# Kernel optimization log

Hardware: AMD Instinct MI355X
Metric: run time of the kernel (lower is better)

Reference implementation:

```python
import jax, jax.numpy as jnp
import numpy as np
import math

D_MODEL = 64
N_HEAD = 8
BATCH = 16
NTOK = 511  # pads to 512 in original torch code; padn = 1 > 0


def setup_inputs() -> dict:
    key = jax.random.key(0)
    ks = jax.random.split(key, 4)
    scl = 0.005
    x = jax.random.normal(ks[0], (BATCH, NTOK, D_MODEL), jnp.float32)
    wq_w = scl * jax.random.normal(ks[1], (N_HEAD * D_MODEL, D_MODEL + 1), jnp.float32)
    wq_w = wq_w.at[:, -1].set(0.0)  # bias column zeroed at init
    wv_w = scl * jax.random.normal(ks[2], (N_HEAD * D_MODEL, D_MODEL + 1), jnp.float32)
    wv_w = wv_w.at[:, -1].set(0.0)
    wk = scl * jnp.ones((N_HEAD, D_MODEL), jnp.float32)
    fanout_w = scl * jax.random.normal(ks[3], (D_MODEL, D_MODEL + 1), jnp.float32)
    fanout_w = fanout_w.at[:, -1].set(0.0)
    return {"x": x, "wq_w": wq_w, "wv_w": wv_w, "wk": wk, "fanout_w": fanout_w}


def _linear_m(w, x):
    # LinearM: w[:, :-1] is weight, w[:, -1] is bias
    return jnp.einsum('oi,bti->bto', w[:, :-1], x) + w[:, -1]


def _l1_logits(q, k):
    # q, k: [b, t, h, w]. Returns [b, s(key), d(query), h] =
    #   -(1/sqrt(w)) * sum_w |q[b,d,h,w] - k[b,s,h,w]|
    # Scan over the width axis so we never materialize a [b,t,t,h,w] tensor.
    b, t, h, w = q.shape
    scale = 1.0 / math.sqrt(w)
    qw = jnp.moveaxis(q, -1, 0)  # [w, b, t, h]
    kw = jnp.moveaxis(k, -1, 0)

    def body(acc, qk):
        qi, ki = qk  # each [b, t, h]
        return acc + jnp.abs(qi[:, None, :, :] - ki[:, :, None, :]), None

    acc0 = jnp.zeros((b, t, t, h), q.dtype)
    acc, _ = jax.lax.scan(body, acc0, (qw, kw))
    return -acc * scale


def reference(x, wq_w, wv_w, wk, fanout_w):
    b, t, dm = x.shape
    q = _linear_m(wq_w, x).reshape(b, t, N_HEAD, D_MODEL)
    v = _linear_m(wv_w, x).reshape(b, t, N_HEAD, D_MODEL)
    # k: x broadcast over heads, elementwise-gated by wk
    k = x[:, :, None, :] * wk[None, None, :, :]  # [b, t, h, w]
    logits = _l1_logits(q, k)  # [b, s, d, h]
    # Extra zero-logit 'sink' key row (the original zero-padded row with a[:,t,:,:]=0)
    sink = jnp.zeros((b, 1, t, N_HEAD), logits.dtype)
    logits = jnp.concatenate([logits, sink], axis=1)  # [b, t+1, d, h]
    a = jax.nn.softmax(logits, axis=1)[:, :t]  # softmax over keys+sink, drop sink
    # einsum 'bsdh,bshw->bdhw' then sum over h, fused:
    out = jnp.einsum('bsdh,bshw->bdw', a, v)  # [b, t, d_model]
    y = jax.nn.relu(out)  # module's self.gelu is actually nn.ReLU()
    y = _linear_m(fanout_w, y)
    return x + y
```

## Files before the change

kernel.cpp:

```cpp
#include <hip/hip_runtime.h>
#include <stdint.h>


#define B  16
#define H  8
#define T  511

typedef __fp16 f16x2 __attribute__((ext_vector_type(2)));
typedef __fp16 f16x8 __attribute__((ext_vector_type(8)));
typedef float  f32x4 __attribute__((ext_vector_type(4)));

#if __has_builtin(__builtin_amdgcn_exp2f)
#define EXP2F(x) __builtin_amdgcn_exp2f(x)
#else
#define EXP2F(x) exp2f(x)
#endif

__device__ __forceinline__ uint32_t SAD(uint32_t a, uint32_t b, uint32_t c) {
#if __has_builtin(__builtin_amdgcn_sad_u8)
  return __builtin_amdgcn_sad_u8(a, b, c);
#else
  uint32_t d;
  asm("v_sad_u8 %0, %1, %2, %3" : "=v"(d) : "v"(a), "v"(b), "v"(c));
  return d;
#endif
}

__device__ __forceinline__ uint32_t PKRTZ(float a, float b) {
  f16x2 r = __builtin_amdgcn_cvt_pkrtz(a, b);
  return __builtin_bit_cast(uint32_t, r);
}

__device__ __forceinline__ uint32_t quantu8(float v) {
  float q = __builtin_rintf(__builtin_fmaf(v, 256.f, 128.f));
  q = fminf(fmaxf(q, 0.f), 255.f);
  return (uint32_t)(int)q;
}

__global__ void wtrans_kernel(const float* __restrict__ wq, const float* __restrict__ wv,
                              const float* __restrict__ wf, float* __restrict__ wt,
                              float* __restrict__ bias, float* __restrict__ wft,
                              float* __restrict__ biasf) {
  const int idx = blockIdx.x * 256 + (int)threadIdx.x;
  if (idx < 64 * 1024) {
    const int k = idx >> 10, j = idx & 1023;
    const float* src = (j < 512) ? wq : wv;
    const int oc = j & 511;
    wt[idx] = src[oc * 65 + k];
    if (k == 0) bias[j] = src[oc * 65 + 64];
  } else if (idx < 64 * 1024 + 64 * 64) {
    const int r = idx - 64 * 1024;
    const int k = r >> 6, w = r & 63;
    wft[r] = wf[w * 65 + k];
    if (k == 0) biasf[w] = wf[w * 65 + 64];
  }
}

__global__ void __launch_bounds__(256, 2) proj_kernel(
    const float* __restrict__ x, const float* __restrict__ wt,
    const float* __restrict__ bias, const float* __restrict__ wk,
    uint8_t* __restrict__ qq, _Float16* __restrict__ vt,
    uint8_t* __restrict__ kq) {
  __shared__ float xt[64][16];
  const int b = blockIdx.y, tc = blockIdx.x;
  const int t0 = tc * 16;
  const int tid = threadIdx.x;
  {
    const int tl = tid >> 4, k0 = (tid & 15) * 4;
    const int t = t0 + tl;
    float4 v = {0.f, 0.f, 0.f, 0.f};
    if (t < T) v = *(const float4*)(x + ((size_t)b * T + t) * 64 + k0);
    xt[k0 + 0][tl] = v.x; xt[k0 + 1][tl] = v.y;
    xt[k0 + 2][tl] = v.z; xt[k0 + 3][tl] = v.w;
  }
  __syncthreads();
  const int j0 = tid * 4;
  const float4 bs = *(const float4*)(bias + j0);
  float4 acc[16];
#pragma unroll
  for (int t = 0; t < 16; ++t) acc[t] = bs;
  for (int k = 0; k < 64; ++k) {
    const float4 w4 = *(const float4*)(wt + (size_t)k * 1024 + j0);
    const float4* xr = (const float4*)xt[k];
    const float4 xa = xr[0], xb = xr[1], xc = xr[2], xd = xr[3];
    const float xv[16] = {xa.x, xa.y, xa.z, xa.w, xb.x, xb.y, xb.z, xb.w,
                          xc.x, xc.y, xc.z, xc.w, xd.x, xd.y, xd.z, xd.w};
#pragma unroll
    for (int t = 0; t < 16; ++t) {
      acc[t].x = __builtin_fmaf(w4.x, xv[t], acc[t].x);
      acc[t].y = __builtin_fmaf(w4.y, xv[t], acc[t].y);
      acc[t].z = __builtin_fmaf(w4.z, xv[t], acc[t].z);
      acc[t].w = __builtin_fmaf(w4.w, xv[t], acc[t].w);
    }
  }
  const int oc = j0 & 511;
  const int hh = oc >> 6, w0 = oc & 63;
  const size_t bh = (size_t)b * H + hh;
  if (j0 < 512) {
#pragma unroll
    for (int t = 0; t < 16; ++t) {
      if (t0 + t < T) {
        const uint32_t u = quantu8(acc[t].x) | (quantu8(acc[t].y) << 8) |
                           (quantu8(acc[t].z) << 16) | (quantu8(acc[t].w) << 24);
        *(uint32_t*)(qq + (bh * T + (size_t)(t0 + t)) * 64 + w0) = u;
      }
    }
  } else {
#pragma unroll
    for (int i = 0; i < 4; ++i) {
      uint32_t u[8];
      const float* a = (const float*)acc;
#pragma unroll
      for (int m = 0; m < 8; ++m) u[m] = PKRTZ(a[4 * (2 * m) + i], a[4 * (2 * m + 1) + i]);
      _Float16* p = vt + (bh * 64 + (size_t)(w0 + i)) * 512 + t0;
      *(uint4*)(p)     = make_uint4(u[0], u[1], u[2], u[3]);
      *(uint4*)(p + 8) = make_uint4(u[4], u[5], u[6], u[7]);
    }
  }
  const int tk = tid >> 4, w4 = (tid & 15) * 4;
  if (t0 + tk < T) {
    const float xv0 = xt[w4 + 0][tk], xv1 = xt[w4 + 1][tk];
    const float xv2 = xt[w4 + 2][tk], xv3 = xt[w4 + 3][tk];
#pragma unroll
    for (int hh2 = 0; hh2 < H; ++hh2) {
      const float4 wkv = *(const float4*)(wk + hh2 * 64 + w4);
      const uint32_t u = quantu8(xv0 * wkv.x) | (quantu8(xv1 * wkv.y) << 8) |
                         (quantu8(xv2 * wkv.z) << 16) | (quantu8(xv3 * wkv.w) << 24);
      *(uint32_t*)(kq + (((size_t)b * H + hh2) * T + (size_t)(t0 + tk)) * 64 + w4) = u;
    }
  }
}

__global__ void __launch_bounds__(256, 1) attn_kernel(
    const uint8_t* __restrict__ qq, const uint8_t* __restrict__ kq,
    const _Float16* __restrict__ vt, _Float16* __restrict__ anum) {
  __shared__ uint4 klds[2048];
  const int qt = blockIdx.x, h = blockIdx.y, b = blockIdx.z;
  const int bh = b * H + h;
  const int tid = threadIdx.x;
  {
    const uint4* kg = (const uint4*)(kq + (size_t)bh * T * 64);
    for (int i = tid; i < T * 4; i += 256) {
      const int s = i >> 2, j = i & 3;
      klds[s * 4 + (j ^ ((s >> 3) & 3))] = kg[i];
    }
  }
  const int wave = tid >> 6, lane = tid & 63;
  const int c = lane & 15, g = lane >> 4;
  const int qb = qt * 256 + wave * 64;
  uint4 q[4][4];
#pragma unroll
  for (int m = 0; m < 4; ++m) {
    const int qm = qb + 16 * m + c;
    const int qsafe = qm < T ? qm : T - 1;
    const uint4* qp = (const uint4*)(qq + ((size_t)bh * T + qsafe) * 64);
#pragma unroll
    for (int i = 0; i < 4; ++i) q[m][i] = qp[i];
  }
  const _Float16* vb = vt + (size_t)bh * 64 * 512;
  f32x4 acc[4][4];
#pragma unroll
  for (int m = 0; m < 4; ++m)
#pragma unroll
    for (int nt = 0; nt < 4; ++nt) acc[m][nt] = f32x4{0.f, 0.f, 0.f, 0.f};
  float den[4] = {0.f, 0.f, 0.f, 0.f};
  const float Cl = -0x1.715476p+0f / 2048.0f;
  __syncthreads();

#pragma unroll 1
  for (int kt = 0; kt < 16; ++kt) {
    const int ks = kt * 32;
    const _Float16* vp0 = vb + (size_t)c * 512 + ks + g * 8;
    uint4 bvec[4];
#pragma unroll
    for (int nt = 0; nt < 4; ++nt) bvec[nt] = *(const uint4*)(vp0 + nt * 16 * 512);
    uint32_t pk[4][4];
#pragma unroll
    for (int jj = 0; jj < 4; ++jj) {
      float pp[4][2];
#pragma unroll
      for (int e = 0; e < 2; ++e) {
        const int s = ks + g * 8 + jj * 2 + e;
        const int sr = s < T ? s : T - 1;
        const uint4* kp = klds + sr * 4;
        const int bb = (sr >> 3) & 3;
        const uint4 k0 = kp[bb], k1 = kp[1 ^ bb], k2 = kp[2 ^ bb], k3 = kp[3 ^ bb];
        const bool live = s < T;
#pragma unroll
        for (int m = 0; m < 4; ++m) {
          uint32_t a0 = 0, a1 = 0;
          a0 = SAD(q[m][0].x, k0.x, a0); a0 = SAD(q[m][0].y, k0.y, a0);
          a0 = SAD(q[m][0].z, k0.z, a0); a0 = SAD(q[m][0].w, k0.w, a0);
          a0 = SAD(q[m][1].x, k1.x, a0); a0 = SAD(q[m][1].y, k1.y, a0);
          a0 = SAD(q[m][1].z, k1.z, a0); a0 = SAD(q[m][1].w, k1.w, a0);
          a1 = SAD(q[m][2].x, k2.x, a1); a1 = SAD(q[m][2].y, k2.y, a1);
          a1 = SAD(q[m][2].z, k2.z, a1); a1 = SAD(q[m][2].w, k2.w, a1);
          a1 = SAD(q[m][3].x, k3.x, a1); a1 = SAD(q[m][3].y, k3.y, a1);
          a1 = SAD(q[m][3].z, k3.z, a1); a1 = SAD(q[m][3].w, k3.w, a1);
          const float p = EXP2F((float)(a0 + a1) * Cl);
          pp[m][e] = live ? p : 0.f;
        }
      }
#pragma unroll
      for (int m = 0; m < 4; ++m) {
        den[m] += pp[m][0] + pp[m][1];
        pk[m][jj] = PKRTZ(pp[m][0], pp[m][1]);
      }
    }
#pragma unroll
    for (int m = 0; m < 4; ++m) {
      const f16x8 af = __builtin_bit_cast(f16x8, make_uint4(pk[m][0], pk[m][1], pk[m][2], pk[m][3]));
#pragma unroll
      for (int nt = 0; nt < 4; ++nt) {
        const f16x8 bf = __builtin_bit_cast(f16x8, bvec[nt]);
        acc[m][nt] = __builtin_amdgcn_mfma_f32_16x16x32_f16(af, bf, acc[m][nt], 0, 0, 0);
      }
    }
  }

#pragma unroll
  for (int m = 0; m < 4; ++m) {
    den[m] += __shfl_xor(den[m], 16, 64);
    den[m] += __shfl_xor(den[m], 32, 64);
    den[m] += 1.0f;
  }
#pragma unroll
  for (int m = 0; m < 4; ++m) {
#pragma unroll
    for (int r = 0; r < 4; ++r) {
      const float rd = 1.0f / __shfl(den[m], g * 4 + r, 64);
      const int qr = qb + 16 * m + g * 4 + r;
      if (qr < T) {
        _Float16* ap = anum + (((size_t)b * T + qr) * H + h) * 64 + c;
        ap[0]  = (_Float16)(acc[m][0][r] * rd);
        ap[16] = (_Float16)(acc[m][1][r] * rd);
        ap[32] = (_Float16)(acc[m][2][r] * rd);
        ap[48] = (_Float16)(acc[m][3][r] * rd);
      }
    }
  }
}

__global__ void __launch_bounds__(256) finalize_kernel(
    const float* __restrict__ x, const _Float16* __restrict__ anum,
    const float* __restrict__ wft, const float* __restrict__ biasf,
    float* __restrict__ out) {
  __shared__ float u[4][64];
  const int tid = threadIdx.x;
  const int lt = tid >> 6, w = tid & 63;
  const int gt = blockIdx.x * 4 + lt;
  const _Float16* an = anum + (size_t)gt * H * 64 + w;
  float s = 0.f;
#pragma unroll
  for (int hh = 0; hh < H; ++hh) s += (float)an[hh * 64];
  u[lt][w] = fmaxf(s, 0.f);
  __syncthreads();
  float y = biasf[w];
#pragma unroll 8
  for (int k = 0; k < 64; ++k) y = __builtin_fmaf(wft[k * 64 + w], u[lt][k], y);
  out[(size_t)gt * 64 + w] = x[(size_t)gt * 64 + w] + y;
}

extern "C" void kernel_launch(void* const* d_in, const int* in_sizes, int n_in,
                              void* d_out, int out_size, void* d_ws, size_t ws_size,
                              hipStream_t stream) {
  (void)in_sizes; (void)n_in; (void)out_size; (void)ws_size;
  const float* x  = (const float*)d_in[0];
  const float* wq = (const float*)d_in[1];
  const float* wv = (const float*)d_in[2];
  const float* wk = (const float*)d_in[3];
  const float* wf = (const float*)d_in[4];
  float* out = (float*)d_out;

  uint8_t* ws = (uint8_t*)d_ws;
  const size_t o_qq   = 0;
  const size_t o_kq   = 4186112;
  const size_t o_vt   = 8372224;
  const size_t o_anum = 16760832;
  const size_t o_wt   = 25133056;
  const size_t o_bias = 25395200;
  const size_t o_wft  = 25399296;
  const size_t o_bf   = 25415680;

  uint8_t*  qq    = ws + o_qq;
  uint8_t*  kq    = ws + o_kq;
  _Float16* vt    = (_Float16*)(ws + o_vt);
  _Float16* anum  = (_Float16*)(ws + o_anum);
  float*    wt    = (float*)(ws + o_wt);
  float*    bias  = (float*)(ws + o_bias);
  float*    wft   = (float*)(ws + o_wft);
  float*    biasf = (float*)(ws + o_bf);

  wtrans_kernel<<<dim3((64 * 1024 + 64 * 64 + 255) / 256), 256, 0, stream>>>(
      wq, wv, wf, wt, bias, wft, biasf);
  proj_kernel<<<dim3(32, B), 256, 0, stream>>>(x, wt, bias, wk, qq, vt, kq);
  attn_kernel<<<dim3(2, H, B), 256, 0, stream>>>(qq, kq, vt, anum);
  finalize_kernel<<<dim3(B * T / 4), 256, 0, stream>>>(x, anum, wft, biasf, out);
}
```

Before: 76.52 us.

## Split attention key range across two wave groups with LDS partial-sum reduction

Doubles the attention block to 512 threads. Two wave groups handle the same query rows, each over half of the key range, and their partial numerators and denominators are combined through LDS. The grid is only 256 blocks on a machine with many CUs, so each CU had just 4 waves; this raises the wave count per block so more latency can be hidden. In exchange it adds an LDS reduction, two extra barriers, and fp16 rounding of the partial accumulators.

New measurement: 77.97 us. No clear change (+1.9%).

```diff
diff --git a/kernel.cpp b/kernel.cpp
--- a/kernel.cpp
+++ b/kernel.cpp
@@ -131,23 +131,25 @@
   }
 }
 
-__global__ void __launch_bounds__(256, 1) attn_kernel(
+__global__ void __launch_bounds__(512, 2) attn_kernel(
     const uint8_t* __restrict__ qq, const uint8_t* __restrict__ kq,
     const _Float16* __restrict__ vt, _Float16* __restrict__ anum) {
   __shared__ uint4 klds[2048];
+  __shared__ float dend[4][4][16];
   const int qt = blockIdx.x, h = blockIdx.y, b = blockIdx.z;
   const int bh = b * H + h;
   const int tid = threadIdx.x;
   {
     const uint4* kg = (const uint4*)(kq + (size_t)bh * T * 64);
-    for (int i = tid; i < T * 4; i += 256) {
+    for (int i = tid; i < T * 4; i += 512) {
       const int s = i >> 2, j = i & 3;
       klds[s * 4 + (j ^ ((s >> 3) & 3))] = kg[i];
     }
   }
   const int wave = tid >> 6, lane = tid & 63;
+  const int pair = wave & 3, khalf = wave >> 2;
   const int c = lane & 15, g = lane >> 4;
-  const int qb = qt * 256 + wave * 64;
+  const int qb = qt * 256 + pair * 64;
   uint4 q[4][4];
 #pragma unroll
   for (int m = 0; m < 4; ++m) {
@@ -168,8 +170,8 @@
   __syncthreads();
 
 #pragma unroll 1
-  for (int kt = 0; kt < 16; ++kt) {
-    const int ks = kt * 32;
+  for (int kt = 0; kt < 8; ++kt) {
+    const int ks = khalf * 256 + kt * 32;
     const _Float16* vp0 = vb + (size_t)c * 512 + ks + g * 8;
     uint4 bvec[4];
 #pragma unroll
@@ -222,20 +224,51 @@
   for (int m = 0; m < 4; ++m) {
     den[m] += __shfl_xor(den[m], 16, 64);
     den[m] += __shfl_xor(den[m], 32, 64);
-    den[m] += 1.0f;
-  }
-#pragma unroll
-  for (int m = 0; m < 4; ++m) {
-#pragma unroll
-    for (int r = 0; r < 4; ++r) {
-      const float rd = 1.0f / __shfl(den[m], g * 4 + r, 64);
-      const int qr = qb + 16 * m + g * 4 + r;
-      if (qr < T) {
-        _Float16* ap = anum + (((size_t)b * T + qr) * H + h) * 64 + c;
-        ap[0]  = (_Float16)(acc[m][0][r] * rd);
-        ap[16] = (_Float16)(acc[m][1][r] * rd);
-        ap[32] = (_Float16)(acc[m][2][r] * rd);
-        ap[48] = (_Float16)(acc[m][3][r] * rd);
+  }
+
+  __syncthreads();
+  uint32_t* scr = (uint32_t*)klds;
+  if (khalf) {
+#pragma unroll
+    for (int m = 0; m < 4; ++m) {
+      if (g == 0) dend[pair][m][c] = den[m];
+#pragma unroll
+      for (int nt = 0; nt < 4; ++nt) {
+        const int j = m * 8 + nt * 2;
+        scr[j * 256 + pair * 64 + lane]       = PKRTZ(acc[m][nt][0], acc[m][nt][1]);
+        scr[(j + 1) * 256 + pair * 64 + lane] = PKRTZ(acc[m][nt][2], acc[m][nt][3]);
+      }
+    }
+  }
+  __syncthreads();
+  if (!khalf) {
+    float dtot[4];
+#pragma unroll
+    for (int m = 0; m < 4; ++m) dtot[m] = den[m] + dend[pair][m][c] + 1.0f;
+#pragma unroll
+    for (int m = 0; m < 4; ++m) {
+#pragma unroll
+      for (int nt = 0; nt < 4; ++nt) {
+        const int j = m * 8 + nt * 2;
+        const f16x2 u0 = __builtin_bit_cast(f16x2, scr[j * 256 + pair * 64 + lane]);
+        const f16x2 u1 = __builtin_bit_cast(f16x2, scr[(j + 1) * 256 + pair * 64 + lane]);
+        acc[m][nt][0] += (float)u0[0]; acc[m][nt][1] += (float)u0[1];
+        acc[m][nt][2] += (float)u1[0]; acc[m][nt][3] += (float)u1[1];
+      }
+    }
+#pragma unroll
+    for (int m = 0; m < 4; ++m) {
+#pragma unroll
+      for (int r = 0; r < 4; ++r) {
+        const float rd = 1.0f / __shfl(dtot[m], g * 4 + r, 64);
+        const int qr = qb + 16 * m + g * 4 + r;
+        if (qr < T) {
+          _Float16* ap = anum + (((size_t)b * T + qr) * H + h) * 64 + c;
+          ap[0]  = (_Float16)(acc[m][0][r] * rd);
+          ap[16] = (_Float16)(acc[m][1][r] * rd);
+          ap[32] = (_Float16)(acc[m][2][r] * rd);
+          ap[48] = (_Float16)(acc[m][3][r] * rd);
+        }
       }
     }
   }
@@ -294,6 +327,6 @@
   wtrans_kernel<<<dim3((64 * 1024 + 64 * 64 + 255) / 256), 256, 0, stream>>>(
       wq, wv, wf, wt, bias, wft, biasf);
   proj_kernel<<<dim3(32, B), 256, 0, stream>>>(x, wt, bias, wk, qq, vt, kq);
-  attn_kernel<<<dim3(2, H, B), 256, 0, stream>>>(qq, kq, vt, anum);
+  attn_kernel<<<dim3(2, H, B), 512, 0, stream>>>(qq, kq, vt, anum);
   finalize_kernel<<<dim3(B * T / 4), 256, 0, stream>>>(x, anum, wft, biasf, out);
 }
```

## Split attention over key halves and smaller query tiles, combine in finalize

Applied to the files above, without the earlier changes.

The attention kernel now launches four times as many blocks. Each block handles 128 queries against one half of the keys, with a smaller register footprint and a higher launch-bounds occupancy hint. Unnormalized partial numerators and denominators are written per key half, and the finalize kernel sums them and applies the softmax normalization. This targets low occupancy and poor CU utilization from the old 256-block grid. In exchange it writes twice as much intermediate data and adds extra reads in finalize. Since the logits are bounded and need no running max, the split-K combination stays exact apart from fp16 rounding of the partial sums.

Measured after the change: 81.39 us. +6.4%, slower.

```diff
diff --git a/kernel.cpp b/kernel.cpp
--- a/kernel.cpp
+++ b/kernel.cpp
@@ -131,26 +131,30 @@
   }
 }
 
-__global__ void __launch_bounds__(256, 1) attn_kernel(
+__global__ void __launch_bounds__(256, 4) attn_kernel(
     const uint8_t* __restrict__ qq, const uint8_t* __restrict__ kq,
-    const _Float16* __restrict__ vt, _Float16* __restrict__ anum) {
-  __shared__ uint4 klds[2048];
-  const int qt = blockIdx.x, h = blockIdx.y, b = blockIdx.z;
+    const _Float16* __restrict__ vt, _Float16* __restrict__ anum0,
+    _Float16* __restrict__ anum1, float* __restrict__ denp) {
+  __shared__ uint4 klds[1024];
+  const int bx = blockIdx.x, h = blockIdx.y, b = blockIdx.z;
+  const int qt = bx & 3, kh = bx >> 2;
   const int bh = b * H + h;
   const int tid = threadIdx.x;
+  const int kbeg = kh * 256;
+  const int nk = kh ? (T - 256) : 256;
   {
-    const uint4* kg = (const uint4*)(kq + (size_t)bh * T * 64);
-    for (int i = tid; i < T * 4; i += 256) {
+    const uint4* kg = (const uint4*)(kq + ((size_t)bh * T + kbeg) * 64);
+    for (int i = tid; i < nk * 4; i += 256) {
       const int s = i >> 2, j = i & 3;
       klds[s * 4 + (j ^ ((s >> 3) & 3))] = kg[i];
     }
   }
   const int wave = tid >> 6, lane = tid & 63;
   const int c = lane & 15, g = lane >> 4;
-  const int qb = qt * 256 + wave * 64;
-  uint4 q[4][4];
-#pragma unroll
-  for (int m = 0; m < 4; ++m) {
+  const int qb = qt * 128 + wave * 32;
+  uint4 q[2][4];
+#pragma unroll
+  for (int m = 0; m < 2; ++m) {
     const int qm = qb + 16 * m + c;
     const int qsafe = qm < T ? qm : T - 1;
     const uint4* qp = (const uint4*)(qq + ((size_t)bh * T + qsafe) * 64);
@@ -158,36 +162,36 @@
     for (int i = 0; i < 4; ++i) q[m][i] = qp[i];
   }
   const _Float16* vb = vt + (size_t)bh * 64 * 512;
-  f32x4 acc[4][4];
-#pragma unroll
-  for (int m = 0; m < 4; ++m)
+  f32x4 acc[2][4];
+#pragma unroll
+  for (int m = 0; m < 2; ++m)
 #pragma unroll
     for (int nt = 0; nt < 4; ++nt) acc[m][nt] = f32x4{0.f, 0.f, 0.f, 0.f};
-  float den[4] = {0.f, 0.f, 0.f, 0.f};
+  float den[2] = {0.f, 0.f};
   const float Cl = -0x1.715476p+0f / 2048.0f;
   __syncthreads();
 
 #pragma unroll 1
-  for (int kt = 0; kt < 16; ++kt) {
-    const int ks = kt * 32;
-    const _Float16* vp0 = vb + (size_t)c * 512 + ks + g * 8;
+  for (int kt = 0; kt < 8; ++kt) {
+    const int s0 = kbeg + kt * 32;
+    const _Float16* vp0 = vb + (size_t)c * 512 + s0 + g * 8;
     uint4 bvec[4];
 #pragma unroll
     for (int nt = 0; nt < 4; ++nt) bvec[nt] = *(const uint4*)(vp0 + nt * 16 * 512);
-    uint32_t pk[4][4];
+    uint32_t pk[2][4];
 #pragma unroll
     for (int jj = 0; jj < 4; ++jj) {
-      float pp[4][2];
+      float pp[2][2];
 #pragma unroll
       for (int e = 0; e < 2; ++e) {
-        const int s = ks + g * 8 + jj * 2 + e;
-        const int sr = s < T ? s : T - 1;
-        const uint4* kp = klds + sr * 4;
-        const int bb = (sr >> 3) & 3;
+        const int s = s0 + g * 8 + jj * 2 + e;
+        const int sl = (s < T ? s : T - 1) - kbeg;
+        const uint4* kp = klds + sl * 4;
+        const int bb = (sl >> 3) & 3;
         const uint4 k0 = kp[bb], k1 = kp[1 ^ bb], k2 = kp[2 ^ bb], k3 = kp[3 ^ bb];
         const bool live = s < T;
 #pragma unroll
-        for (int m = 0; m < 4; ++m) {
+        for (int m = 0; m < 2; ++m) {
           uint32_t a0 = 0, a1 = 0;
           a0 = SAD(q[m][0].x, k0.x, a0); a0 = SAD(q[m][0].y, k0.y, a0);
           a0 = SAD(q[m][0].z, k0.z, a0); a0 = SAD(q[m][0].w, k0.w, a0);
@@ -202,13 +206,13 @@
         }
       }
 #pragma unroll
-      for (int m = 0; m < 4; ++m) {
+      for (int m = 0; m < 2; ++m) {
         den[m] += pp[m][0] + pp[m][1];
         pk[m][jj] = PKRTZ(pp[m][0], pp[m][1]);
       }
     }
 #pragma unroll
-    for (int m = 0; m < 4; ++m) {
+    for (int m = 0; m < 2; ++m) {
       const f16x8 af = __builtin_bit_cast(f16x8, make_uint4(pk[m][0], pk[m][1], pk[m][2], pk[m][3]));
 #pragma unroll
       for (int nt = 0; nt < 4; ++nt) {
@@ -219,40 +223,56 @@
   }
 
 #pragma unroll
-  for (int m = 0; m < 4; ++m) {
+  for (int m = 0; m < 2; ++m) {
     den[m] += __shfl_xor(den[m], 16, 64);
     den[m] += __shfl_xor(den[m], 32, 64);
-    den[m] += 1.0f;
-  }
-#pragma unroll
-  for (int m = 0; m < 4; ++m) {
+  }
+  if (g == 0) {
+#pragma unroll
+    for (int m = 0; m < 2; ++m) {
+      const int qd = qb + 16 * m + c;
+      if (qd < T) denp[(size_t)kh * (B * T * H) + ((size_t)b * T + qd) * H + h] = den[m];
+    }
+  }
+  _Float16* abase = kh ? anum1 : anum0;
+#pragma unroll
+  for (int m = 0; m < 2; ++m) {
 #pragma unroll
     for (int r = 0; r < 4; ++r) {
-      const float rd = 1.0f / __shfl(den[m], g * 4 + r, 64);
       const int qr = qb + 16 * m + g * 4 + r;
       if (qr < T) {
-        _Float16* ap = anum + (((size_t)b * T + qr) * H + h) * 64 + c;
-        ap[0]  = (_Float16)(acc[m][0][r] * rd);
-        ap[16] = (_Float16)(acc[m][1][r] * rd);
-        ap[32] = (_Float16)(acc[m][2][r] * rd);
-        ap[48] = (_Float16)(acc[m][3][r] * rd);
+        _Float16* ap = abase + (((size_t)b * T + qr) * H + h) * 64 + c;
+        ap[0]  = (_Float16)acc[m][0][r];
+        ap[16] = (_Float16)acc[m][1][r];
+        ap[32] = (_Float16)acc[m][2][r];
+        ap[48] = (_Float16)acc[m][3][r];
       }
     }
   }
 }
 
 __global__ void __launch_bounds__(256) finalize_kernel(
-    const float* __restrict__ x, const _Float16* __restrict__ anum,
+    const float* __restrict__ x, const _Float16* __restrict__ anum0,
+    const _Float16* __restrict__ anum1, const float* __restrict__ denp,
     const float* __restrict__ wft, const float* __restrict__ biasf,
     float* __restrict__ out) {
   __shared__ float u[4][64];
+  __shared__ float rd[4][8];
   const int tid = threadIdx.x;
   const int lt = tid >> 6, w = tid & 63;
   const int gt = blockIdx.x * 4 + lt;
-  const _Float16* an = anum + (size_t)gt * H * 64 + w;
+  if (w < 8) {
+    const float d0 = denp[(size_t)gt * H + w];
+    const float d1 = denp[(size_t)(B * T * H) + (size_t)gt * H + w];
+    rd[lt][w] = 1.0f / (d0 + d1 + 1.0f);
+  }
+  __syncthreads();
+  const _Float16* p0 = anum0 + (size_t)gt * H * 64 + w;
+  const _Float16* p1 = anum1 + (size_t)gt * H * 64 + w;
   float s = 0.f;
 #pragma unroll
-  for (int hh = 0; hh < H; ++hh) s += (float)an[hh * 64];
+  for (int hh = 0; hh < H; ++hh)
+    s += ((float)p0[hh * 64] + (float)p1[hh * 64]) * rd[lt][hh];
   u[lt][w] = fmaxf(s, 0.f);
   __syncthreads();
   float y = biasf[w];
@@ -276,16 +296,20 @@
   const size_t o_qq   = 0;
   const size_t o_kq   = 4186112;
   const size_t o_vt   = 8372224;
-  const size_t o_anum = 16760832;
-  const size_t o_wt   = 25133056;
-  const size_t o_bias = 25395200;
-  const size_t o_wft  = 25399296;
-  const size_t o_bf   = 25415680;
+  const size_t o_a0   = 16760832;
+  const size_t o_a1   = 25133056;
+  const size_t o_den  = 33505280;
+  const size_t o_wt   = 34028544;
+  const size_t o_bias = 34290688;
+  const size_t o_wft  = 34294784;
+  const size_t o_bf   = 34311168;
 
   uint8_t*  qq    = ws + o_qq;
   uint8_t*  kq    = ws + o_kq;
   _Float16* vt    = (_Float16*)(ws + o_vt);
-  _Float16* anum  = (_Float16*)(ws + o_anum);
+  _Float16* a0    = (_Float16*)(ws + o_a0);
+  _Float16* a1    = (_Float16*)(ws + o_a1);
+  float*    denp  = (float*)(ws + o_den);
   float*    wt    = (float*)(ws + o_wt);
   float*    bias  = (float*)(ws + o_bias);
   float*    wft   = (float*)(ws + o_wft);
@@ -294,6 +318,6 @@
   wtrans_kernel<<<dim3((64 * 1024 + 64 * 64 + 255) / 256), 256, 0, stream>>>(
       wq, wv, wf, wt, bias, wft, biasf);
   proj_kernel<<<dim3(32, B), 256, 0, stream>>>(x, wt, bias, wk, qq, vt, kq);
-  attn_kernel<<<dim3(2, H, B), 256, 0, stream>>>(qq, kq, vt, anum);
-  finalize_kernel<<<dim3(B * T / 4), 256, 0, stream>>>(x, anum, wft, biasf, out);
-}
+  attn_kernel<<<dim3(8, H, B), 256, 0, stream>>>(qq, kq, vt, a0, a1, denp);
+  finalize_kernel<<<dim3(B * T / 4), 256, 0, stream>>>(x, a0, a1, denp, wft, biasf, out);
+}
```

## Split attention keys across waves with per-lane queries and LDS reduction

Applied to the files above, without the earlier changes.

The attention kernel now gives each block 64 queries, one per lane, and splits the 512 keys across the four waves. K is read with wave-uniform addresses from global memory instead of being staged in LDS. The probability tiles are transposed through LDS to form MFMA operands, and the per-wave partial outputs and denominators are reduced through LDS at the end. The grid grows from 256 to 1024 blocks and launch bounds allow 4 blocks per CU to raise occupancy, at the cost of an extra LDS transpose and a cross-wave reduction. The proj kernel's k loop is also partially unrolled.

Result: slower. 142.4 us (+86.1%).

```diff
diff --git a/kernel.cpp b/kernel.cpp
--- a/kernel.cpp
+++ b/kernel.cpp
@@ -79,6 +79,7 @@
   float4 acc[16];
 #pragma unroll
   for (int t = 0; t < 16; ++t) acc[t] = bs;
+#pragma unroll 4
   for (int k = 0; k < 64; ++k) {
     const float4 w4 = *(const float4*)(wt + (size_t)k * 1024 + j0);
     const float4* xr = (const float4*)xt[k];
@@ -131,85 +132,75 @@
   }
 }
 
-__global__ void __launch_bounds__(256, 1) attn_kernel(
+__global__ void __launch_bounds__(256, 4) attn_kernel(
     const uint8_t* __restrict__ qq, const uint8_t* __restrict__ kq,
     const _Float16* __restrict__ vt, _Float16* __restrict__ anum) {
-  __shared__ uint4 klds[2048];
+  __shared__ uint32_t lbuf[8704 + 256];
   const int qt = blockIdx.x, h = blockIdx.y, b = blockIdx.z;
   const int bh = b * H + h;
   const int tid = threadIdx.x;
-  {
-    const uint4* kg = (const uint4*)(kq + (size_t)bh * T * 64);
-    for (int i = tid; i < T * 4; i += 256) {
-      const int s = i >> 2, j = i & 3;
-      klds[s * 4 + (j ^ ((s >> 3) & 3))] = kg[i];
-    }
-  }
   const int wave = tid >> 6, lane = tid & 63;
   const int c = lane & 15, g = lane >> 4;
-  const int qb = qt * 256 + wave * 64;
-  uint4 q[4][4];
-#pragma unroll
-  for (int m = 0; m < 4; ++m) {
-    const int qm = qb + 16 * m + c;
-    const int qsafe = qm < T ? qm : T - 1;
+  const int qb = qt * 64;
+  const int q = qb + lane;
+  const int qsafe = q < T ? q : T - 1;
+  uint4 q4[4];
+  {
     const uint4* qp = (const uint4*)(qq + ((size_t)bh * T + qsafe) * 64);
 #pragma unroll
-    for (int i = 0; i < 4; ++i) q[m][i] = qp[i];
+    for (int i = 0; i < 4; ++i) q4[i] = qp[i];
   }
   const _Float16* vb = vt + (size_t)bh * 64 * 512;
+  const uint8_t* kqb = kq + (size_t)bh * T * 64;
+  uint32_t* tp = lbuf + wave * (16 * 68);
   f32x4 acc[4][4];
 #pragma unroll
   for (int m = 0; m < 4; ++m)
 #pragma unroll
     for (int nt = 0; nt < 4; ++nt) acc[m][nt] = f32x4{0.f, 0.f, 0.f, 0.f};
-  float den[4] = {0.f, 0.f, 0.f, 0.f};
+  float den = 0.f;
   const float Cl = -0x1.715476p+0f / 2048.0f;
-  __syncthreads();
+  const int wbase = wave * 128;
 
 #pragma unroll 1
-  for (int kt = 0; kt < 16; ++kt) {
-    const int ks = kt * 32;
-    const _Float16* vp0 = vb + (size_t)c * 512 + ks + g * 8;
+  for (int kt = 0; kt < 4; ++kt) {
+    const int s0 = wbase + kt * 32;
+    const uint32_t koff = (uint32_t)__builtin_amdgcn_readfirstlane(s0 * 64);
+    const uint4* kp = (const uint4*)(kqb + koff);
+    const _Float16* vp0 = vb + (size_t)c * 512 + s0 + g * 8;
     uint4 bvec[4];
 #pragma unroll
     for (int nt = 0; nt < 4; ++nt) bvec[nt] = *(const uint4*)(vp0 + nt * 16 * 512);
-    uint32_t pk[4][4];
-#pragma unroll
-    for (int jj = 0; jj < 4; ++jj) {
-      float pp[4][2];
-#pragma unroll
-      for (int e = 0; e < 2; ++e) {
-        const int s = ks + g * 8 + jj * 2 + e;
-        const int sr = s < T ? s : T - 1;
-        const uint4* kp = klds + sr * 4;
-        const int bb = (sr >> 3) & 3;
-        const uint4 k0 = kp[bb], k1 = kp[1 ^ bb], k2 = kp[2 ^ bb], k3 = kp[3 ^ bb];
-        const bool live = s < T;
-#pragma unroll
-        for (int m = 0; m < 4; ++m) {
-          uint32_t a0 = 0, a1 = 0;
-          a0 = SAD(q[m][0].x, k0.x, a0); a0 = SAD(q[m][0].y, k0.y, a0);
-          a0 = SAD(q[m][0].z, k0.z, a0); a0 = SAD(q[m][0].w, k0.w, a0);
-          a0 = SAD(q[m][1].x, k1.x, a0); a0 = SAD(q[m][1].y, k1.y, a0);
-          a0 = SAD(q[m][1].z, k1.z, a0); a0 = SAD(q[m][1].w, k1.w, a0);
-          a1 = SAD(q[m][2].x, k2.x, a1); a1 = SAD(q[m][2].y, k2.y, a1);
-          a1 = SAD(q[m][2].z, k2.z, a1); a1 = SAD(q[m][2].w, k2.w, a1);
-          a1 = SAD(q[m][3].x, k3.x, a1); a1 = SAD(q[m][3].y, k3.y, a1);
-          a1 = SAD(q[m][3].z, k3.z, a1); a1 = SAD(q[m][3].w, k3.w, a1);
-          const float p = EXP2F((float)(a0 + a1) * Cl);
-          pp[m][e] = live ? p : 0.f;
-        }
-      }
-#pragma unroll
-      for (int m = 0; m < 4; ++m) {
-        den[m] += pp[m][0] + pp[m][1];
-        pk[m][jj] = PKRTZ(pp[m][0], pp[m][1]);
-      }
-    }
+    const bool kill = (wbase + 128 > T) && (kt == 3);
+    uint32_t pdw[16];
+    float pprev = 0.f;
+#pragma unroll
+    for (int j = 0; j < 32; ++j) {
+      const uint4 ka = kp[j * 4 + 0], kb_ = kp[j * 4 + 1];
+      const uint4 kc = kp[j * 4 + 2], kd = kp[j * 4 + 3];
+      uint32_t a0 = 0, a1 = 0;
+      a0 = SAD(q4[0].x, ka.x, a0); a0 = SAD(q4[0].y, ka.y, a0);
+      a0 = SAD(q4[0].z, ka.z, a0); a0 = SAD(q4[0].w, ka.w, a0);
+      a0 = SAD(q4[1].x, kb_.x, a0); a0 = SAD(q4[1].y, kb_.y, a0);
+      a0 = SAD(q4[1].z, kb_.z, a0); a0 = SAD(q4[1].w, kb_.w, a0);
+      a1 = SAD(q4[2].x, kc.x, a1); a1 = SAD(q4[2].y, kc.y, a1);
+      a1 = SAD(q4[2].z, kc.z, a1); a1 = SAD(q4[2].w, kc.w, a1);
+      a1 = SAD(q4[3].x, kd.x, a1); a1 = SAD(q4[3].y, kd.y, a1);
+      a1 = SAD(q4[3].z, kd.z, a1); a1 = SAD(q4[3].w, kd.w, a1);
+      float p = EXP2F((float)(a0 + a1) * Cl);
+      if (kill && j == 31) p = 0.f;
+      den += p;
+      if (j & 1) pdw[j >> 1] = PKRTZ(pprev, p); else pprev = p;
+    }
+#pragma unroll
+    for (int d = 0; d < 16; ++d) tp[d * 68 + lane] = pdw[d];
 #pragma unroll
     for (int m = 0; m < 4; ++m) {
-      const f16x8 af = __builtin_bit_cast(f16x8, make_uint4(pk[m][0], pk[m][1], pk[m][2], pk[m][3]));
+      const uint32_t r0 = tp[(g * 4 + 0) * 68 + m * 16 + c];
+      const uint32_t r1 = tp[(g * 4 + 1) * 68 + m * 16 + c];
+      const uint32_t r2 = tp[(g * 4 + 2) * 68 + m * 16 + c];
+      const uint32_t r3 = tp[(g * 4 + 3) * 68 + m * 16 + c];
+      const f16x8 af = __builtin_bit_cast(f16x8, make_uint4(r0, r1, r2, r3));
 #pragma unroll
       for (int nt = 0; nt < 4; ++nt) {
         const f16x8 bf = __builtin_bit_cast(f16x8, bvec[nt]);
@@ -218,25 +209,44 @@
     }
   }
 
-#pragma unroll
-  for (int m = 0; m < 4; ++m) {
-    den[m] += __shfl_xor(den[m], 16, 64);
-    den[m] += __shfl_xor(den[m], 32, 64);
-    den[m] += 1.0f;
-  }
-#pragma unroll
-  for (int m = 0; m < 4; ++m) {
-#pragma unroll
-    for (int r = 0; r < 4; ++r) {
-      const float rd = 1.0f / __shfl(den[m], g * 4 + r, 64);
-      const int qr = qb + 16 * m + g * 4 + r;
-      if (qr < T) {
-        _Float16* ap = anum + (((size_t)b * T + qr) * H + h) * 64 + c;
-        ap[0]  = (_Float16)(acc[m][0][r] * rd);
-        ap[16] = (_Float16)(acc[m][1][r] * rd);
-        ap[32] = (_Float16)(acc[m][2][r] * rd);
-        ap[48] = (_Float16)(acc[m][3][r] * rd);
-      }
+  float* dens = (float*)(lbuf + 8704);
+  dens[wave * 64 + lane] = den;
+  __syncthreads();
+  const float dtot = dens[0 * 64 + lane] + dens[1 * 64 + lane] +
+                     dens[2 * 64 + lane] + dens[3 * 64 + lane] + 1.0f;
+  uint32_t* cb = lbuf + wave * 2176;
+#pragma unroll
+  for (int m = 0; m < 4; ++m)
+#pragma unroll
+    for (int nt = 0; nt < 4; ++nt) {
+      const int d0 = m * 8 + nt * 2;
+      cb[d0 * 68 + lane]       = PKRTZ(acc[m][nt][0], acc[m][nt][1]);
+      cb[(d0 + 1) * 68 + lane] = PKRTZ(acc[m][nt][2], acc[m][nt][3]);
+    }
+  __syncthreads();
+  const int m = wave;
+#pragma unroll
+  for (int w = 0; w < 4; ++w) {
+    if (w == wave) continue;
+#pragma unroll
+    for (int nt = 0; nt < 4; ++nt) {
+      const int d0 = m * 8 + nt * 2;
+      const f16x2 u0 = __builtin_bit_cast(f16x2, lbuf[w * 2176 + d0 * 68 + lane]);
+      const f16x2 u1 = __builtin_bit_cast(f16x2, lbuf[w * 2176 + (d0 + 1) * 68 + lane]);
+      acc[m][nt][0] += (float)u0[0]; acc[m][nt][1] += (float)u0[1];
+      acc[m][nt][2] += (float)u1[0]; acc[m][nt][3] += (float)u1[1];
+    }
+  }
+#pragma unroll
+  for (int r = 0; r < 4; ++r) {
+    const float rd = 1.0f / __shfl(dtot, m * 16 + g * 4 + r, 64);
+    const int qr = qb + m * 16 + g * 4 + r;
+    if (qr < T) {
+      _Float16* ap = anum + (((size_t)b * T + qr) * H + h) * 64 + c;
+      ap[0]  = (_Float16)(acc[m][0][r] * rd);
+      ap[16] = (_Float16)(acc[m][1][r] * rd);
+      ap[32] = (_Float16)(acc[m][2][r] * rd);
+      ap[48] = (_Float16)(acc[m][3][r] * rd);
     }
   }
 }
@@ -294,6 +304,6 @@
   wtrans_kernel<<<dim3((64 * 1024 + 64 * 64 + 255) / 256), 256, 0, stream>>>(
       wq, wv, wf, wt, bias, wft, biasf);
   proj_kernel<<<dim3(32, B), 256, 0, stream>>>(x, wt, bias, wk, qq, vt, kq);
-  attn_kernel<<<dim3(2, H, B), 256, 0, stream>>>(qq, kq, vt, anum);
+  attn_kernel<<<dim3(8, H, B), 256, 0, stream>>>(qq, kq, vt, anum);
   finalize_kernel<<<dim3(B * T / 4), 256, 0, stream>>>(x, anum, wft, biasf, out);
 }
```
